# Kernel tuning notes

Hardware: AMD Instinct MI355X
Metric: run time of the kernel (lower is better)

## Reference

```python
import jax, jax.numpy as jnp
import numpy as np

LN_EPS = 1e-5


def setup_inputs() -> dict:
    key = jax.random.key(0)
    ks = jax.random.split(key, 5)
    B, S, DIN, DOUT = 4, 2048, 4096, 4096
    return {
        "x": jax.random.normal(ks[0], (B, S, DIN), dtype=jnp.float32),
        "weight": jax.random.normal(ks[1], (DOUT, DIN), dtype=jnp.float32),
        "in_channel_scale": jax.random.uniform(ks[2], (DIN,), dtype=jnp.float32, minval=0.1, maxval=1.0),
        "out_channel_scale": jax.random.uniform(ks[3], (DOUT,), dtype=jnp.float32, minval=0.1, maxval=1.0),
        "bias": jax.random.normal(ks[4], (DOUT,), dtype=jnp.float32) * 0.02,
        "ln_gamma": jnp.ones((DOUT,), dtype=jnp.float32),
        "ln_beta": jnp.zeros((DOUT,), dtype=jnp.float32),
    }


def reference(x, weight, in_channel_scale, out_channel_scale, bias, ln_gamma, ln_beta):
    # BitNet-style 1-bit quantization of the weight (sign), per-channel scaling.
    w_bin = jnp.sign(weight)  # [out, in], values in {-1, 0, +1}
    # (x * in_scale) @ w_bin.T * out_scale + bias
    h = jnp.einsum('bsi,oi->bso', x * in_channel_scale, w_bin) * out_channel_scale + bias
    # LayerNorm over out_features with learnable affine
    mu = jnp.mean(h, axis=-1, keepdims=True)
    var = jnp.mean(jnp.square(h - mu), axis=-1, keepdims=True)
    h = (h - mu) * jax.lax.rsqrt(var + LN_EPS)
    return h * ln_gamma + ln_beta
```

## Files before the change

### kernel.cpp

```cpp
#include <hip/hip_runtime.h>
#include <hip/hip_bf16.h>

constexpr int GM = 8192;
constexpr int GN = 4096;
constexpr int GK = 4096;

constexpr int BM = 256, BN = 256, BK = 64;
constexpr int NSTEP = GK / BK;
constexpr int SLOT_BYTES = (BM + BN) * BK;
constexpr int LDS_BYTES = 2 * SLOT_BYTES;

constexpr int PX_BLOCKS = GM;
constexpr int PW_BLOCKS = (GN * GK) / (256 * 8);

using bf16x8 = __attribute__((ext_vector_type(8))) __bf16;
using i32x4  = __attribute__((ext_vector_type(4))) int;

__global__ __launch_bounds__(256) void prep_fused_i8(
    const float* __restrict__ x, const float* __restrict__ iscale,
    const float* __restrict__ w, signed char* __restrict__ A,
    signed char* __restrict__ Wb, float* __restrict__ alpha) {
  int b = blockIdx.x;
  int t = threadIdx.x;
  if (b < PX_BLOCKS) {
    int row = b;
    const float* xr = x + (size_t)row * GK;
    float v[16];
    float mx = 0.f;
#pragma unroll
    for (int p = 0; p < 4; ++p) {
      int idx = p * 1024 + t * 4;
      float4 xv = *(const float4*)(xr + idx);
      float4 sv = *(const float4*)(iscale + idx);
      float a0 = xv.x * sv.x, a1 = xv.y * sv.y, a2 = xv.z * sv.z, a3 = xv.w * sv.w;
      v[p * 4 + 0] = a0; v[p * 4 + 1] = a1; v[p * 4 + 2] = a2; v[p * 4 + 3] = a3;
      mx = fmaxf(mx, fmaxf(fmaxf(fabsf(a0), fabsf(a1)), fmaxf(fabsf(a2), fabsf(a3))));
    }
#pragma unroll
    for (int off = 32; off > 0; off >>= 1)
      mx = fmaxf(mx, __shfl_down(mx, off));
    __shared__ float rm[4];
    int wid = t >> 6, lane = t & 63;
    if (lane == 0) rm[wid] = mx;
    __syncthreads();
    float m = fmaxf(fmaxf(rm[0], rm[1]), fmaxf(rm[2], rm[3]));
    float inv = m > 0.f ? 127.f / m : 0.f;
    if (t == 0) alpha[row] = m * (1.f / 127.f);
#pragma unroll
    for (int p = 0; p < 4; ++p) {
      int idx = p * 1024 + t * 4;
      char4 q;
      int q0 = (int)rintf(v[p * 4 + 0] * inv);
      int q1 = (int)rintf(v[p * 4 + 1] * inv);
      int q2 = (int)rintf(v[p * 4 + 2] * inv);
      int q3 = (int)rintf(v[p * 4 + 3] * inv);
      q.x = (signed char)max(-127, min(127, q0));
      q.y = (signed char)max(-127, min(127, q1));
      q.z = (signed char)max(-127, min(127, q2));
      q.w = (signed char)max(-127, min(127, q3));
      *(char4*)(A + (size_t)row * GK + idx) = q;
    }
  } else {
    int e = ((b - PX_BLOCKS) * 256 + t) * 8;
    float4 v0 = *(const float4*)(w + e);
    float4 v1 = *(const float4*)(w + e + 4);
    auto sg = [](float v) -> signed char {
      return (signed char)((v > 0.f) - (v < 0.f));
    };
    union { signed char c[8]; unsigned long long u; } o;
    o.c[0] = sg(v0.x); o.c[1] = sg(v0.y); o.c[2] = sg(v0.z); o.c[3] = sg(v0.w);
    o.c[4] = sg(v1.x); o.c[5] = sg(v1.y); o.c[6] = sg(v1.z); o.c[7] = sg(v1.w);
    *(unsigned long long*)(Wb + e) = o.u;
  }
}

__device__ inline void gload16(const void* g, const void* l) {
  __builtin_amdgcn_global_load_lds(
      (const __attribute__((address_space(1))) void*)g,
      (__attribute__((address_space(3))) void*)l, 16, 0, 0);
}

__global__ __launch_bounds__(512, 2) void gemm_i8(
    const signed char* __restrict__ A, const signed char* __restrict__ Bm,
    const float* __restrict__ alpha, float* __restrict__ C) {
  extern __shared__ signed char lds8[];

  int bid = blockIdx.x;
  int x = bid & 7, idx = bid >> 3;
  int brow = ((x & 3) << 3) | (idx & 7);
  int bcol = ((x >> 2) << 3) | (idx >> 3);

  int tid = threadIdx.x, wid = tid >> 6, lane = tid & 63;
  int wm = wid & 1, wn = wid >> 1;
  int lrow = lane & 15, lkhi = lane >> 4;

  const signed char* Ab = A + (size_t)(brow * BM) * GK;
  const signed char* Bb = Bm + (size_t)(bcol * BN) * GK;

  int rchunk = lkhi ^ ((lrow >> 1) & 3);
  int avbase = (wm * 128 + lrow) * 64 + rchunk * 16;
  int bvbase = 16384 + (wn * 64 + lrow) * 64 + rchunk * 16;

  int grow = tid >> 2;
  int gcol = ((tid & 3) ^ ((tid >> 3) & 3)) * 16;

  auto STAGE = [&](int kstep, int si) {
    const signed char* sA = Ab + (size_t)grow * GK + kstep * BK + gcol;
    const signed char* dA = lds8 + si * SLOT_BYTES + tid * 16;
    gload16(sA, dA);
    gload16(sA + (size_t)128 * GK, dA + 8192);
    const signed char* sB = Bb + (size_t)grow * GK + kstep * BK + gcol;
    gload16(sB, dA + 16384);
    gload16(sB + (size_t)128 * GK, dA + 16384 + 8192);
  };

  i32x4 acc[8][4] = {};

  STAGE(0, 0);
  __syncthreads();

  for (int t = 0; t < NSTEP; ++t) {
    const signed char* sl = lds8 + (t & 1) * SLOT_BYTES;
    if (t + 1 < NSTEP) STAGE(t + 1, (t + 1) & 1);

    i32x4 af[8], bf[4];
#pragma unroll
    for (int mi = 0; mi < 8; ++mi)
      af[mi] = *(const i32x4*)(sl + avbase + mi * 1024);
#pragma unroll
    for (int ni = 0; ni < 4; ++ni)
      bf[ni] = *(const i32x4*)(sl + bvbase + ni * 1024);

#pragma unroll
    for (int mi = 0; mi < 8; ++mi)
#pragma unroll
      for (int ni = 0; ni < 4; ++ni)
        acc[mi][ni] = __builtin_amdgcn_mfma_i32_16x16x64_i8(
            af[mi], bf[ni], acc[mi][ni], 0, 0, 0);

    __syncthreads();
  }

  int crow0 = brow * BM + wm * 128;
  int ccol0 = bcol * BN + wn * 64;
  char* Cb = (char*)C;
#pragma unroll
  for (int mi = 0; mi < 8; ++mi)
#pragma unroll
    for (int ni = 0; ni < 4; ++ni) {
      int col = ccol0 + ni * 16 + lrow;
#pragma unroll
      for (int r = 0; r < 4; ++r) {
        int row = crow0 + mi * 16 + lkhi * 4 + r;
        float h = alpha[row] * (float)acc[mi][ni][r];
        *(__bf16*)(Cb + (size_t)row * 16384 + 8192 + col * 2) = (__bf16)h;
      }
    }
}

__global__ __launch_bounds__(256) void ln_fuse(
    float* __restrict__ out, const float* __restrict__ os,
    const float* __restrict__ bs, const float* __restrict__ g,
    const float* __restrict__ be) {
  constexpr int N = GN;
  int row = blockIdx.x;
  const __bf16* hr = (const __bf16*)((const char*)out + (size_t)row * 16384 + 8192);
  float* orow = out + (size_t)row * N;
  int t = threadIdx.x;

  float v[16];
  float sum = 0.f, ssq = 0.f;
#pragma unroll
  for (int c = 0; c < 2; ++c) {
    int idx = c * 2048 + t * 8;
    bf16x8 hv = *(const bf16x8*)(hr + idx);
    float4 s0 = *(const float4*)(os + idx);
    float4 s1 = *(const float4*)(os + idx + 4);
    float4 b0 = *(const float4*)(bs + idx);
    float4 b1 = *(const float4*)(bs + idx + 4);
#pragma unroll
    for (int j = 0; j < 4; ++j) {
      float a = (float)hv[j] * (&s0.x)[j] + (&b0.x)[j];
      v[c * 8 + j] = a;
      sum += a; ssq += a * a;
    }
#pragma unroll
    for (int j = 0; j < 4; ++j) {
      float a = (float)hv[4 + j] * (&s1.x)[j] + (&b1.x)[j];
      v[c * 8 + 4 + j] = a;
      sum += a; ssq += a * a;
    }
  }

#pragma unroll
  for (int off = 32; off > 0; off >>= 1) {
    sum += __shfl_down(sum, off);
    ssq += __shfl_down(ssq, off);
  }
  __shared__ float rs[8];
  int wid = t >> 6, lane = t & 63;
  if (lane == 0) { rs[wid] = sum; rs[4 + wid] = ssq; }
  __syncthreads();
  sum = rs[0] + rs[1] + rs[2] + rs[3];
  ssq = rs[4] + rs[5] + rs[6] + rs[7];

  float mean = sum * (1.f / N);
  float var = ssq * (1.f / N) - mean * mean;
  float rstd = rsqrtf(var + 1e-5f);

#pragma unroll
  for (int c = 0; c < 2; ++c) {
    int idx = c * 2048 + t * 8;
    float4 g0 = *(const float4*)(g + idx);
    float4 g1 = *(const float4*)(g + idx + 4);
    float4 e0 = *(const float4*)(be + idx);
    float4 e1 = *(const float4*)(be + idx + 4);
    float4 o0, o1;
#pragma unroll
    for (int j = 0; j < 4; ++j) {
      (&o0.x)[j] = (v[c * 8 + j] - mean) * rstd * (&g0.x)[j] + (&e0.x)[j];
      (&o1.x)[j] = (v[c * 8 + 4 + j] - mean) * rstd * (&g1.x)[j] + (&e1.x)[j];
    }
    *(float4*)(orow + idx) = o0;
    *(float4*)(orow + idx + 4) = o1;
  }
}

extern "C" void kernel_launch(void* const* d_in, const int* in_sizes, int n_in,
                              void* d_out, int out_size, void* d_ws, size_t ws_size,
                              hipStream_t stream) {
  const float* x      = (const float*)d_in[0];
  const float* w      = (const float*)d_in[1];
  const float* iscale = (const float*)d_in[2];
  const float* oscale = (const float*)d_in[3];
  const float* bias   = (const float*)d_in[4];
  const float* gamma  = (const float*)d_in[5];
  const float* beta   = (const float*)d_in[6];
  float* out = (float*)d_out;

  signed char* Ai8 = (signed char*)d_ws;
  signed char* Wi8 = (signed char*)d_ws + (size_t)GM * GK;
  float* alpha = (float*)((char*)d_ws + (size_t)GM * GK + (size_t)GN * GK);

  (void)hipFuncSetAttribute((const void*)gemm_i8,
                            hipFuncAttributeMaxDynamicSharedMemorySize, LDS_BYTES);

  prep_fused_i8<<<PX_BLOCKS + PW_BLOCKS, 256, 0, stream>>>(x, iscale, w, Ai8,
                                                           Wi8, alpha);
  gemm_i8<<<(GM / BM) * (GN / BN), 512, LDS_BYTES, stream>>>(Ai8, Wi8, alpha, out);
  ln_fuse<<<GM, 256, 0, stream>>>(out, oscale, bias, gamma, beta);
}
```

Before: 213.2 us.

## Pre-swizzle binary weights into MFMA fragment order and load B directly to registers

The weight-prep kernel now writes the sign-quantized weights in a fragment-major layout that matches the 16x16x64 i8 MFMA operand order. The GEMM then loads B fragments straight from global memory into registers, double-buffered across two k-steps, and only stages A through LDS. This halves LDS traffic and footprint, which could raise occupancy. In exchange, each wave issues redundant global loads for B (the two wm waves read the same fragments), and global-load latency is now exposed in the register pipeline.

```diff
diff --git a/kernel.cpp b/kernel.cpp
--- a/kernel.cpp
+++ b/kernel.cpp
@@ -7,11 +7,11 @@
 
 constexpr int BM = 256, BN = 256, BK = 64;
 constexpr int NSTEP = GK / BK;
-constexpr int SLOT_BYTES = (BM + BN) * BK;
+constexpr int SLOT_BYTES = BM * BK;
 constexpr int LDS_BYTES = 2 * SLOT_BYTES;
 
 constexpr int PX_BLOCKS = GM;
-constexpr int PW_BLOCKS = (GN * GK) / (256 * 8);
+constexpr int PW_BLOCKS = (GN * GK / 16) / 256;
 
 using bf16x8 = __attribute__((ext_vector_type(8))) __bf16;
 using i32x4  = __attribute__((ext_vector_type(4))) int;
@@ -19,7 +19,7 @@
 __global__ __launch_bounds__(256) void prep_fused_i8(
     const float* __restrict__ x, const float* __restrict__ iscale,
     const float* __restrict__ w, signed char* __restrict__ A,
-    signed char* __restrict__ Wb, float* __restrict__ alpha) {
+    signed char* __restrict__ Wf, float* __restrict__ alpha) {
   int b = blockIdx.x;
   int t = threadIdx.x;
   if (b < PX_BLOCKS) {
@@ -61,16 +61,22 @@
       *(char4*)(A + (size_t)row * GK + idx) = q;
     }
   } else {
-    int e = ((b - PX_BLOCKS) * 256 + t) * 8;
-    float4 v0 = *(const float4*)(w + e);
-    float4 v1 = *(const float4*)(w + e + 4);
-    auto sg = [](float v) -> signed char {
-      return (signed char)((v > 0.f) - (v < 0.f));
+    int T = (b - PX_BLOCKS) * 256 + t;
+    int lane = T & 63, ks = (T >> 6) & 63, rt = T >> 12;
+    const float* src = w + (size_t)(rt * 16 + (lane & 15)) * GK
+                         + ks * 64 + (lane >> 4) * 16;
+    auto sg = [](float v) -> unsigned int {
+      return v > 0.f ? 1u : (v < 0.f ? 0xFFu : 0u);
     };
-    union { signed char c[8]; unsigned long long u; } o;
-    o.c[0] = sg(v0.x); o.c[1] = sg(v0.y); o.c[2] = sg(v0.z); o.c[3] = sg(v0.w);
-    o.c[4] = sg(v1.x); o.c[5] = sg(v1.y); o.c[6] = sg(v1.z); o.c[7] = sg(v1.w);
-    *(unsigned long long*)(Wb + e) = o.u;
+    int4 o;
+    unsigned int r[4];
+#pragma unroll
+    for (int qi = 0; qi < 4; ++qi) {
+      float4 vv = *(const float4*)(src + qi * 4);
+      r[qi] = sg(vv.x) | (sg(vv.y) << 8) | (sg(vv.z) << 16) | (sg(vv.w) << 24);
+    }
+    o.x = (int)r[0]; o.y = (int)r[1]; o.z = (int)r[2]; o.w = (int)r[3];
+    *(int4*)(Wf + (size_t)T * 16) = o;
   }
 }
 
@@ -81,7 +87,7 @@
 }
 
 __global__ __launch_bounds__(512, 2) void gemm_i8(
-    const signed char* __restrict__ A, const signed char* __restrict__ Bm,
+    const signed char* __restrict__ A, const signed char* __restrict__ Wf,
     const float* __restrict__ alpha, float* __restrict__ C) {
   extern __shared__ signed char lds8[];
 
@@ -95,50 +101,65 @@
   int lrow = lane & 15, lkhi = lane >> 4;
 
   const signed char* Ab = A + (size_t)(brow * BM) * GK;
-  const signed char* Bb = Bm + (size_t)(bcol * BN) * GK;
+  const signed char* Bw = Wf + ((size_t)(bcol * 16 + wn * 4) * 64 * 64 + lane) * 16;
 
   int rchunk = lkhi ^ ((lrow >> 1) & 3);
   int avbase = (wm * 128 + lrow) * 64 + rchunk * 16;
-  int bvbase = 16384 + (wn * 64 + lrow) * 64 + rchunk * 16;
 
   int grow = tid >> 2;
   int gcol = ((tid & 3) ^ ((tid >> 3) & 3)) * 16;
 
-  auto STAGE = [&](int kstep, int si) {
+  auto STAGE_A = [&](int kstep, int si) {
     const signed char* sA = Ab + (size_t)grow * GK + kstep * BK + gcol;
     const signed char* dA = lds8 + si * SLOT_BYTES + tid * 16;
     gload16(sA, dA);
     gload16(sA + (size_t)128 * GK, dA + 8192);
-    const signed char* sB = Bb + (size_t)grow * GK + kstep * BK + gcol;
-    gload16(sB, dA + 16384);
-    gload16(sB + (size_t)128 * GK, dA + 16384 + 8192);
   };
 
+  i32x4 bvA[4], bvB[4];
+  auto LOADB = [&](int u, i32x4 (&bv)[4]) {
+#pragma unroll
+    for (int ni = 0; ni < 4; ++ni)
+      bv[ni] = *(const i32x4*)(Bw + ((size_t)ni * 64 + u) * 1024);
+  };
+
   i32x4 acc[8][4] = {};
 
-  STAGE(0, 0);
+  STAGE_A(0, 0);
+  LOADB(0, bvA);
   __syncthreads();
 
-  for (int t = 0; t < NSTEP; ++t) {
-    const signed char* sl = lds8 + (t & 1) * SLOT_BYTES;
-    if (t + 1 < NSTEP) STAGE(t + 1, (t + 1) & 1);
-
-    i32x4 af[8], bf[4];
-#pragma unroll
-    for (int mi = 0; mi < 8; ++mi)
-      af[mi] = *(const i32x4*)(sl + avbase + mi * 1024);
-#pragma unroll
-    for (int ni = 0; ni < 4; ++ni)
-      bf[ni] = *(const i32x4*)(sl + bvbase + ni * 1024);
-
-#pragma unroll
-    for (int mi = 0; mi < 8; ++mi)
-#pragma unroll
-      for (int ni = 0; ni < 4; ++ni)
-        acc[mi][ni] = __builtin_amdgcn_mfma_i32_16x16x64_i8(
-            af[mi], bf[ni], acc[mi][ni], 0, 0, 0);
-
-    __syncthreads();
+  for (int t = 0; t < NSTEP; t += 2) {
+    {
+      const signed char* sl = lds8 + (t & 1) * SLOT_BYTES;
+      if (t + 1 < NSTEP) { STAGE_A(t + 1, (t + 1) & 1); LOADB(t + 1, bvB); }
+      i32x4 af[8];
+#pragma unroll
+      for (int mi = 0; mi < 8; ++mi)
+        af[mi] = *(const i32x4*)(sl + avbase + mi * 1024);
+#pragma unroll
+      for (int mi = 0; mi < 8; ++mi)
+#pragma unroll
+        for (int ni = 0; ni < 4; ++ni)
+          acc[mi][ni] = __builtin_amdgcn_mfma_i32_16x16x64_i8(
+              af[mi], bvA[ni], acc[mi][ni], 0, 0, 0);
+      __syncthreads();
+    }
+    {
+      const signed char* sl = lds8 + ((t + 1) & 1) * SLOT_BYTES;
+      if (t + 2 < NSTEP) { STAGE_A(t + 2, (t + 2) & 1); LOADB(t + 2, bvA); }
+      i32x4 af[8];
+#pragma unroll
+      for (int mi = 0; mi < 8; ++mi)
+        af[mi] = *(const i32x4*)(sl + avbase + mi * 1024);
+#pragma unroll
+      for (int mi = 0; mi < 8; ++mi)
+#pragma unroll
+        for (int ni = 0; ni < 4; ++ni)
+          acc[mi][ni] = __builtin_amdgcn_mfma_i32_16x16x64_i8(
+              af[mi], bvB[ni], acc[mi][ni], 0, 0, 0);
+      if (t + 2 < NSTEP) __syncthreads();
+    }
   }
 
   int crow0 = brow * BM + wm * 128;
@@ -239,14 +260,14 @@
   float* out = (float*)d_out;
 
   signed char* Ai8 = (signed char*)d_ws;
-  signed char* Wi8 = (signed char*)d_ws + (size_t)GM * GK;
+  signed char* Wf  = (signed char*)d_ws + (size_t)GM * GK;
   float* alpha = (float*)((char*)d_ws + (size_t)GM * GK + (size_t)GN * GK);
 
   (void)hipFuncSetAttribute((const void*)gemm_i8,
                             hipFuncAttributeMaxDynamicSharedMemorySize, LDS_BYTES);
 
   prep_fused_i8<<<PX_BLOCKS + PW_BLOCKS, 256, 0, stream>>>(x, iscale, w, Ai8,
-                                                           Wi8, alpha);
-  gemm_i8<<<(GM / BM) * (GN / BN), 512, LDS_BYTES, stream>>>(Ai8, Wi8, alpha, out);
+                                                           Wf, alpha);
+  gemm_i8<<<(GM / BM) * (GN / BN), 512, LDS_BYTES, stream>>>(Ai8, Wf, alpha, out);
   ln_fuse<<<GM, 256, 0, stream>>>(out, oscale, bias, gamma, beta);
 }
```

Result: slower. 224.5 us (+5.3%).
